# Optimization experiments

Hardware: AMD Instinct MI355X
Metric: run time of the kernel (lower is better)

The kernel has to match this reference:

```python
import jax, jax.numpy as jnp
import numpy as np

HEADS = 8
DIM_HEAD = 64
CHUNK = 128
EPS = 1e-6
KERNEL_EPS = 1e-4


def softmax_kernel(x, proj, is_query):
    # x: [b,h,n,d], proj: [f,d]  (FAVOR+ positive softmax features)
    d = x.shape[-1]
    data_normalizer = d ** -0.25
    ratio = proj.shape[0] ** -0.5
    data_dash = jnp.einsum('bhnd,fd->bhnf', x * data_normalizer, proj)
    diag = 0.5 * (data_normalizer ** 2) * jnp.sum(x * x, axis=-1, keepdims=True)  # [b,h,n,1]
    if is_query:
        m = jnp.max(data_dash, axis=-1, keepdims=True)
    else:
        m = jnp.max(data_dash, axis=(-1, -2), keepdims=True)
    return ratio * (jnp.exp(data_dash - diag - jax.lax.stop_gradient(m)) + KERNEL_EPS)


def infer_hidden_states(q, k, v, chunk_size=CHUNK):
    # q,k: [b,h,n,f], v: [b,h,n,e]; chunked causal linear attention with carried cumsums
    b, h, n, f = q.shape
    e = v.shape[-1]
    nc = n // chunk_size

    def to_chunks(t):
        return jnp.moveaxis(t.reshape(b, h, nc, chunk_size, t.shape[-1]), 2, 0)

    qs, ks, vs = to_chunks(q), to_chunks(k), to_chunks(v)

    def step(carry, inp):
        Z, S = carry  # [b,h,1,f], [b,h,1,f,e]
        qc, kc, vc = inp
        k_cum = Z + jnp.cumsum(kc, axis=2)                       # [b,h,c,f]
        D_inv = 1.0 / jnp.einsum('bhnf,bhnf->bhn', qc, k_cum + EPS)
        ctx = jnp.einsum('bhnf,bhne->bhnfe', kc, vc)             # [b,h,c,f,e]
        ctx_cum = S + jnp.cumsum(ctx, axis=2)
        out = jnp.einsum('bhnfe,bhnf,bhn->bhne', ctx_cum, qc, D_inv)
        return (k_cum[:, :, -1:], ctx_cum[:, :, -1:]), out

    init = (jnp.zeros((b, h, 1, f), q.dtype), jnp.zeros((b, h, 1, f, e), q.dtype))
    (Z, S), outs = jax.lax.scan(step, init, (qs, ks, vs))
    out = jnp.moveaxis(outs, 0, 2).reshape(b, h, n, e)
    return out, Z[:, :, 0], S[:, :, 0]


def reference(x, proj, Wq, Wk, Wv, Wo, bo):
    b, n, dim = x.shape
    h, dh = HEADS, DIM_HEAD

    def split_heads(t):
        return jnp.transpose(t.reshape(b, n, h, dh), (0, 2, 1, 3))

    q = split_heads(x @ Wq)
    k = split_heads(x @ Wk)
    v = split_heads(x @ Wv)

    qf = softmax_kernel(q, proj, is_query=True)
    kf = softmax_kernel(k, proj, is_query=False)

    out, Z, S = infer_hidden_states(qf, kf, v)
    out = jnp.transpose(out, (0, 2, 1, 3)).reshape(b, n, h * dh)
    out = out @ Wo + bo
    return out, Z, S


def setup_inputs() -> dict:
    key = jax.random.key(0)
    ks = jax.random.split(key, 6)
    b, n, dim = 2, 2048, 512
    f = 256
    return {
        'x': jax.random.normal(ks[0], (b, n, dim), jnp.float32),
        'proj': jax.random.normal(ks[1], (f, DIM_HEAD), jnp.float32),
        'Wq': jax.random.normal(ks[2], (dim, dim), jnp.float32) * (dim ** -0.5),
        'Wk': jax.random.normal(ks[3], (dim, dim), jnp.float32) * (dim ** -0.5),
        'Wv': jax.random.normal(ks[4], (dim, dim), jnp.float32) * (dim ** -0.5),
        'Wo': jax.random.normal(ks[5], (dim, dim), jnp.float32) * (dim ** -0.5),
        'bo': jnp.zeros((dim,), jnp.float32),
    }
```

## Files before the change

### kernel.cpp

```cpp
#include <hip/hip_runtime.h>
#include <hip/hip_bf16.h>
#include <math.h>

#define NB    2
#define NSEQ  2048
#define DIMM  512
#define NH    8
#define DHd   64
#define FF    256
#define CHK   128
#define NCHK  16
#define NBH   16

typedef unsigned short ushort_t;
typedef __attribute__((ext_vector_type(8))) __bf16 bf16x8;
typedef __attribute__((ext_vector_type(4))) float floatx4;

__device__ __forceinline__ unsigned short f2bf(float x) {
    union { __hip_bfloat16 h; unsigned short u; } v;
    v.h = __float2bfloat16(x);
    return v.u;
}
__device__ __forceinline__ float bf2f(unsigned short u) {
    union { unsigned short u2[2]; float f; } v;
    v.u2[0] = 0; v.u2[1] = u;
    return v.f;
}
__device__ __forceinline__ unsigned enc_f(float x) {
    unsigned u = __float_as_uint(x);
    return (u & 0x80000000u) ? ~u : (u | 0x80000000u);
}
__device__ __forceinline__ float dec_f(unsigned e) {
    unsigned u = (e & 0x80000000u) ? (e & 0x7fffffffu) : ~e;
    return __uint_as_float(u);
}

__device__ __forceinline__ void gload16(const void* g, void* l) {
    __builtin_amdgcn_global_load_lds(
        (const __attribute__((address_space(1))) void*)g,
        (__attribute__((address_space(3))) void*)l, 16, 0, 0);
}

__device__ __forceinline__ bf16x8 frag8(const ushort_t* lds, int row, int kb) {
    return *((const bf16x8*)lds + row * 8 + (kb ^ (row & 7)));
}
__device__ __forceinline__ bf16x8 fragS(const ushort_t* lds, int row, int kb) {
    return *((const bf16x8*)lds + row * 16 + (kb ^ (row & 15)));
}

__device__ __forceinline__ void stage8(const ushort_t* __restrict__ G, ushort_t* dst,
                                       int ld, int tid) {
#pragma unroll
    for (int t = 0; t < 4; t++) {
        const int g = t * 256 + tid, r = g >> 3, kb = (g & 7) ^ (r & 7);
        gload16(G + (size_t)r * ld + kb * 8, dst + (size_t)g * 8);
    }
}
__device__ __forceinline__ void stage4h(const ushort_t* __restrict__ G, ushort_t* dst,
                                        int ld, int tid) {
#pragma unroll
    for (int t = 0; t < 2; t++) {
        const int g = t * 256 + tid, r = g >> 3, kb = (g & 7) ^ (r & 7);
        gload16(G + (size_t)r * ld + kb * 8, dst + (size_t)g * 8);
    }
}
__device__ __forceinline__ void stageV(const ushort_t* __restrict__ G, ushort_t* dst,
                                       int tid) {
#pragma unroll
    for (int t = 0; t < 4; t++) {
        const int g = t * 256 + tid, r = g >> 4, kb = (g & 15) ^ (r & 15);
        gload16(G + (size_t)r * NSEQ + kb * 8, dst + (size_t)g * 8);
    }
}

__global__ __launch_bounds__(256)
void prep(const float* __restrict__ x, const float* __restrict__ proj,
          const float* __restrict__ W0, const float* __restrict__ W1,
          const float* __restrict__ W2, const float* __restrict__ W3,
          ushort_t* __restrict__ xb, ushort_t* __restrict__ projb,
          ushort_t* __restrict__ T0, ushort_t* __restrict__ T1,
          ushort_t* __restrict__ T2, ushort_t* __restrict__ T3,
          unsigned* __restrict__ mk_u)
{
    __shared__ float t[32][33];
    const int b = blockIdx.x, tid = threadIdx.x;
    if (b < 2048) {
        const int gid = b * 256 + tid;
        const float4 v = *(const float4*)(x + (size_t)gid * 4);
        union { ushort4 v4; unsigned short s[4]; } pk;
        pk.s[0] = f2bf(v.x); pk.s[1] = f2bf(v.y); pk.s[2] = f2bf(v.z); pk.s[3] = f2bf(v.w);
        ((ushort4*)xb)[gid] = pk.v4;
    } else if (b < 2064) {
        const int gid = (b - 2048) * 256 + tid;
        const float dn = 0.35355339059327379f;
        const float4 v = *(const float4*)(proj + (size_t)gid * 4);
        union { ushort4 v4; unsigned short s[4]; } pk;
        pk.s[0] = f2bf(v.x * dn); pk.s[1] = f2bf(v.y * dn);
        pk.s[2] = f2bf(v.z * dn); pk.s[3] = f2bf(v.w * dn);
        ((ushort4*)projb)[gid] = pk.v4;
    } else if (b < 3088) {
        const int idx = b - 2064;
        const int z = idx >> 8, rem = idx & 255;
        const int bx = rem & 15, by = rem >> 4;
        const float* W = (z == 0) ? W0 : (z == 1) ? W1 : (z == 2) ? W2 : W3;
        ushort_t* T = (z == 0) ? T0 : (z == 1) ? T1 : (z == 2) ? T2 : T3;
        const int x0 = bx * 32, y0 = by * 32;
        const int tx = tid & 31, ty = tid >> 5;
#pragma unroll
        for (int i = 0; i < 4; i++)
            t[ty + i * 8][tx] = W[(size_t)(y0 + ty + i * 8) * DIMM + x0 + tx];
        __syncthreads();
#pragma unroll
        for (int i = 0; i < 4; i++)
            T[(size_t)(x0 + ty + i * 8) * DIMM + y0 + tx] = f2bf(t[tx][ty + i * 8]);
    } else {
        if (tid < NBH) mk_u[tid] = 0u;
    }
}

__device__ __forceinline__ void mfma_mainloop(
    const ushort_t* __restrict__ AG, const ushort_t* __restrict__ BG,
    ushort_t* As, ushort_t* Bs, int ldA, int ldB, int K,
    floatx4 acc[4][4], int tid)
{
    const int lane = tid & 63, wid = tid >> 6;
    const int q = lane >> 4, c = lane & 15;
    const int wm = (wid >> 1) * 64, wn = (wid & 1) * 64;

    for (int k0 = 0; k0 < K; k0 += 64) {
#pragma unroll
        for (int t = 0; t < 4; t++) {
            const int g = t * 256 + tid, r = g >> 3, kb = (g & 7) ^ (r & 7);
            gload16(AG + (size_t)r * ldA + k0 + kb * 8, As + (size_t)g * 8);
        }
#pragma unroll
        for (int t = 0; t < 4; t++) {
            const int g = t * 256 + tid, r = g >> 3, kb = (g & 7) ^ (r & 7);
            gload16(BG + (size_t)r * ldB + k0 + kb * 8, Bs + (size_t)g * 8);
        }
        __syncthreads();
#pragma unroll
        for (int ks = 0; ks < 2; ks++) {
            bf16x8 af[4], bfr[4];
#pragma unroll
            for (int i = 0; i < 4; i++) {
                af[i]  = frag8(As, wm + i * 16 + c, ks * 4 + q);
                bfr[i] = frag8(Bs, wn + i * 16 + c, ks * 4 + q);
            }
#pragma unroll
            for (int i = 0; i < 4; i++)
#pragma unroll
                for (int j = 0; j < 4; j++)
                    acc[i][j] = __builtin_amdgcn_mfma_f32_16x16x32_bf16(
                        af[i], bfr[j], acc[i][j], 0, 0, 0);
        }
        __syncthreads();
    }
}

__global__ __launch_bounds__(256)
void gemm_qkv(const ushort_t* __restrict__ xb,
              const ushort_t* __restrict__ Wtq, const ushort_t* __restrict__ Wtk,
              const ushort_t* __restrict__ Wtv, const ushort_t* __restrict__ projb,
              ushort_t* __restrict__ qb, ushort_t* __restrict__ kb,
              ushort_t* __restrict__ vTb, unsigned* __restrict__ mk_u)
{
    __shared__ alignas(16) ushort_t SM[25600];
    __shared__ float red[256];
    ushort_t* As = SM;
    ushort_t* Bs = SM + 8192;
    ushort_t* PS = SM + 17408;
    const int tid = threadIdx.x;
    const int bid = blockIdx.x;
    const int z = bid % 3, tt = bid / 3;
    const int n0 = (tt & 3) * 128, m0 = (tt >> 2) * 128;
    const ushort_t* Bt = (z == 0) ? Wtq : ((z == 1) ? Wtk : Wtv);

    floatx4 zero = {0.f, 0.f, 0.f, 0.f};
    floatx4 acc[4][4];
#pragma unroll
    for (int i = 0; i < 4; i++)
#pragma unroll
        for (int j = 0; j < 4; j++) acc[i][j] = zero;

    mfma_mainloop(xb + (size_t)m0 * DIMM, Bt + (size_t)n0 * DIMM, As, Bs,
                  DIMM, DIMM, DIMM, acc, tid);

    const int lane = tid & 63, wid = tid >> 6;
    const int q = lane >> 4, cl = lane & 15;
    const int wm = (wid >> 1) * 64, wn = (wid & 1) * 64;

#pragma unroll
    for (int i = 0; i < 4; i++)
#pragma unroll
        for (int j = 0; j < 4; j++) {
            const int col = wn + j * 16 + cl;
#pragma unroll
            for (int r = 0; r < 4; r++) {
                const int row = wm + i * 16 + q * 4 + r;
                SM[row * 136 + col] = f2bf(acc[i][j][r]);
            }
        }
    __syncthreads();

    if (z < 2) {
        ushort_t* ob = (z == 0) ? qb : kb;
        if (z == 1) {
#pragma unroll
            for (int t = 0; t < 4; t++) {
                const int g = t * 256 + tid, f = g >> 3, kbg = (g & 7) ^ (f & 7);
                gload16(projb + (size_t)f * 64 + kbg * 8, PS + (size_t)g * 8);
            }
        }
#pragma unroll
        for (int p = 0; p < 16; p++) {
            const int idx = p * 256 + tid;
            const int row = idx >> 5, c4 = idx & 31;
            ushort4 o = *(const ushort4*)&SM[row * 136 + c4 * 4];
            *(ushort4*)(ob + (size_t)(m0 + row) * DIMM + n0 + c4 * 4) = o;
        }
        if (z == 1) {
            const int bb = m0 >> 11;
            const int h0 = n0 >> 6;
            float mx[2] = {-3.0e38f, -3.0e38f};
#pragma unroll
            for (int half = 0; half < 2; half++) {
                __syncthreads();
#pragma unroll
                for (int hh = 0; hh < 2; hh++) {
                    floatx4 a2[4][4];
#pragma unroll
                    for (int i = 0; i < 4; i++)
#pragma unroll
                        for (int j = 0; j < 4; j++) a2[i][j] = zero;
#pragma unroll
                    for (int ks = 0; ks < 2; ks++) {
                        bf16x8 af[4], bfr[4];
#pragma unroll
                        for (int i = 0; i < 4; i++)
                            af[i] = *(const bf16x8*)&SM[(wm + i * 16 + cl) * 136 + hh * 64 + (ks * 4 + q) * 8];
#pragma unroll
                        for (int j = 0; j < 4; j++)
                            bfr[j] = frag8(PS, wn + j * 16 + cl, ks * 4 + q);
#pragma unroll
                        for (int i = 0; i < 4; i++)
#pragma unroll
                            for (int j = 0; j < 4; j++)
                                a2[i][j] = __builtin_amdgcn_mfma_f32_16x16x32_bf16(
                                    af[i], bfr[j], a2[i][j], 0, 0, 0);
                    }
#pragma unroll
                    for (int i = 0; i < 4; i++)
#pragma unroll
                        for (int j = 0; j < 4; j++)
#pragma unroll
                            for (int r = 0; r < 4; r++) mx[hh] = fmaxf(mx[hh], a2[i][j][r]);
                }
                if (half == 0) {
                    __syncthreads();
#pragma unroll
                    for (int t = 0; t < 4; t++) {
                        const int g = t * 256 + tid, f = g >> 3, kbg = (g & 7) ^ (f & 7);
                        gload16(projb + (size_t)(128 + f) * 64 + kbg * 8, PS + (size_t)g * 8);
                    }
                }
            }
#pragma unroll
            for (int hh = 0; hh < 2; hh++) {
                __syncthreads();
                red[tid] = mx[hh];
                __syncthreads();
                for (int s = 128; s > 0; s >>= 1) {
                    if (tid < s) red[tid] = fmaxf(red[tid], red[tid + s]);
                    __syncthreads();
                }
                if (tid == 0) atomicMax(&mk_u[bb * NH + h0 + hh], enc_f(red[0]));
            }
        }
    } else {
        const int bb = m0 >> 11, nbase = m0 & 2047;
#pragma unroll
        for (int p = 0; p < 16; p++) {
            const int idx = p * 256 + tid;
            const int cl2 = idx >> 5, n4 = idx & 31;
            const int C = n0 + cl2;
            const int h = C >> 6, e = C & 63;
            union { ushort4 v4; unsigned short s[4]; } pk;
#pragma unroll
            for (int k = 0; k < 4; k++) pk.s[k] = SM[(n4 * 4 + k) * 136 + cl2];
            *(ushort4*)(vTb + (((size_t)(bb * NH + h) * 64 + e)) * NSEQ + nbase + n4 * 4) = pk.v4;
        }
    }
}

__global__ __launch_bounds__(256)
void gemm_out(const ushort_t* __restrict__ attnb, const ushort_t* __restrict__ Wto,
              float* __restrict__ out, const float* __restrict__ bias)
{
    __shared__ alignas(16) ushort_t As[4096];
    __shared__ alignas(16) ushort_t Bs[8192];
    const int tid = threadIdx.x;
    const int n0 = blockIdx.x * 128, m0 = blockIdx.y * 64;
    const ushort_t* AG = attnb + (size_t)m0 * DIMM;
    const ushort_t* BG = Wto + (size_t)n0 * DIMM;

    floatx4 zero = {0.f, 0.f, 0.f, 0.f};
    floatx4 acc[2][4];
#pragma unroll
    for (int i = 0; i < 2; i++)
#pragma unroll
        for (int j = 0; j < 4; j++) acc[i][j] = zero;

    const int lane = tid & 63, wid = tid >> 6;
    const int q = lane >> 4, c = lane & 15;
    const int wm = (wid >> 1) * 32, wn = (wid & 1) * 64;

    for (int k0 = 0; k0 < DIMM; k0 += 64) {
        stage4h(AG + k0, As, DIMM, tid);
        stage8(BG + k0, Bs, DIMM, tid);
        __syncthreads();
#pragma unroll
        for (int ks = 0; ks < 2; ks++) {
            bf16x8 af[2], bfr[4];
#pragma unroll
            for (int i = 0; i < 2; i++) af[i] = frag8(As, wm + i * 16 + c, ks * 4 + q);
#pragma unroll
            for (int j = 0; j < 4; j++) bfr[j] = frag8(Bs, wn + j * 16 + c, ks * 4 + q);
#pragma unroll
            for (int i = 0; i < 2; i++)
#pragma unroll
                for (int j = 0; j < 4; j++)
                    acc[i][j] = __builtin_amdgcn_mfma_f32_16x16x32_bf16(
                        af[i], bfr[j], acc[i][j], 0, 0, 0);
        }
        __syncthreads();
    }

#pragma unroll
    for (int i = 0; i < 2; i++)
#pragma unroll
        for (int j = 0; j < 4; j++) {
            const int col = n0 + wn + j * 16 + c;
            const float bv = bias[col];
#pragma unroll
            for (int r = 0; r < 4; r++) {
                const int row = m0 + wm + i * 16 + q * 4 + r;
                out[(size_t)row * DIMM + col] = acc[i][j][r] + bv;
            }
        }
}

__global__ __launch_bounds__(256)
void featk(const ushort_t* __restrict__ kb_, const ushort_t* __restrict__ projb,
           const unsigned* __restrict__ mk_u, const ushort_t* __restrict__ vTb,
           ushort_t* __restrict__ kfb, float* __restrict__ CTXT,
           float* __restrict__ Ksum)
{
    __shared__ alignas(16) ushort_t SM[17408];
    __shared__ alignas(16) ushort_t Vs[8192];
    __shared__ float dtmp[256];
    __shared__ float diag_l[128];
    __shared__ float colp[2][128];
    ushort_t* As = SM;
    ushort_t* Bs = SM + 8192;
    const int tid = threadIdx.x, lane = tid & 63, wid = tid >> 6;
    const int q = lane >> 4, cl = lane & 15;
    const int m0 = blockIdx.x * 128, h = blockIdx.y, fh = blockIdx.z;
    const int bb = m0 >> 11, nloc = m0 & 2047;
    const int bh = bb * NH + h;
    const int cidx = nloc >> 7;
    const ushort_t* Aq = kb_ + (size_t)m0 * DIMM + h * 64;
    const ushort_t* Vg = vTb + ((size_t)bh * 64) * NSEQ + nloc;
    const ushort_t* Pj = projb + (size_t)fh * 128 * 64;

    {
        const int row = tid >> 1, half = tid & 1;
        float s = 0.f;
        const ushort_t* p = Aq + (size_t)row * DIMM + half * 32;
#pragma unroll
        for (int d = 0; d < 32; d += 4) {
            ushort4 w = *(const ushort4*)(p + d);
            float a = bf2f(w.x), b2 = bf2f(w.y), c2 = bf2f(w.z), d2 = bf2f(w.w);
            s += a * a + b2 * b2 + c2 * c2 + d2 * d2;
        }
        dtmp[tid] = s;
    }
    stage8(Aq, As, DIMM, tid);
    stage8(Pj, Bs, 64, tid);
    stageV(Vg, Vs, tid);
    __syncthreads();
    if (tid < 128) diag_l[tid] = (dtmp[2 * tid] + dtmp[2 * tid + 1]) * 0.0625f;

    floatx4 zero = {0.f, 0.f, 0.f, 0.f};
    floatx4 acc[4][4];
#pragma unroll
    for (int i = 0; i < 4; i++)
#pragma unroll
        for (int j = 0; j < 4; j++) acc[i][j] = zero;
    const int wm = (wid >> 1) * 64, wn = (wid & 1) * 64;
#pragma unroll
    for (int ks = 0; ks < 2; ks++) {
        bf16x8 af[4], bfr[4];
#pragma unroll
        for (int i = 0; i < 4; i++) af[i] = frag8(As, wm + i * 16 + cl, ks * 4 + q);
#pragma unroll
        for (int j = 0; j < 4; j++) bfr[j] = frag8(Bs, wn + j * 16 + cl, ks * 4 + q);
#pragma unroll
        for (int i = 0; i < 4; i++)
#pragma unroll
            for (int j = 0; j < 4; j++)
                acc[i][j] = __builtin_amdgcn_mfma_f32_16x16x32_bf16(
                    af[i], bfr[j], acc[i][j], 0, 0, 0);
    }
    __syncthreads();

    const float mk = dec_f(mk_u[bh]);
#pragma unroll
    for (int i = 0; i < 4; i++)
#pragma unroll
        for (int r = 0; r < 4; r++) {
            const int row = wm + i * 16 + q * 4 + r;
            const float cc = diag_l[row] + mk;
#pragma unroll
            for (int j = 0; j < 4; j++)
                acc[i][j][r] = 0.0625f * (__expf(acc[i][j][r] - cc) + 1.0e-4f);
        }

#pragma unroll
    for (int j = 0; j < 4; j++) {
        float s = 0.f;
#pragma unroll
        for (int i = 0; i < 4; i++)
            s += acc[i][j][0] + acc[i][j][1] + acc[i][j][2] + acc[i][j][3];
        s += __shfl_xor(s, 16);
        s += __shfl_xor(s, 32);
        if (q == 0) colp[wid >> 1][wn + j * 16 + cl] = s;
    }

#pragma unroll
    for (int i = 0; i < 4; i++)
#pragma unroll
        for (int j = 0; j < 4; j++) {
            const int col = wn + j * 16 + cl;
#pragma unroll
            for (int r = 0; r < 4; r++) {
                const int row = wm + i * 16 + q * 4 + r;
                SM[row * 136 + col] = f2bf(acc[i][j][r]);
            }
        }
    __syncthreads();

    if (tid < 128)
        Ksum[((size_t)bh * NCHK + cidx) * FF + fh * 128 + tid] = colp[0][tid] + colp[1][tid];

    const size_t frow = (size_t)bh * NSEQ + nloc;
#pragma unroll
    for (int p = 0; p < 16; p++) {
        const int idx = p * 256 + tid;
        const int row = idx >> 5, c4 = idx & 31;
        ushort4 o = *(const ushort4*)&SM[row * 136 + c4 * 4];
        *(ushort4*)(kfb + (frow + row) * FF + fh * 128 + c4 * 4) = o;
    }
    __syncthreads();

    ushort_t* T = SM;
    const size_t cbase = ((size_t)bh * NCHK + cidx) * 64;
#pragma unroll
    for (int fq = 0; fq < 2; fq++) {
        if ((wid & 1) == fq) {
#pragma unroll
            for (int jj = 0; jj < 4; jj++) {
#pragma unroll
                for (int i = 0; i < 4; i++)
#pragma unroll
                    for (int r = 0; r < 4; r++) {
                        const int n = wm + i * 16 + q * 4 + r;
                        T[(jj * 16 + cl) * 136 + n] = f2bf(acc[i][jj][r]);
                    }
            }
        }
        __syncthreads();
        floatx4 accc[4];
#pragma unroll
        for (int jj = 0; jj < 4; jj++) accc[jj] = zero;
#pragma unroll
        for (int kt = 0; kt < 4; kt++) {
            const bf16x8 av = fragS(Vs, wid * 16 + cl, kt * 4 + q);
#pragma unroll
            for (int jj = 0; jj < 4; jj++) {
                const bf16x8 bv = *(const bf16x8*)(T + (jj * 16 + cl) * 136 + (kt * 4 + q) * 8);
                accc[jj] = __builtin_amdgcn_mfma_f32_16x16x32_bf16(av, bv, accc[jj], 0, 0, 0);
            }
        }
#pragma unroll
        for (int jj = 0; jj < 4; jj++) {
            const int f = fh * 128 + fq * 64 + jj * 16 + cl;
#pragma unroll
            for (int r = 0; r < 4; r++) {
                const int e = wid * 16 + q * 4 + r;
                CTXT[(cbase + e) * FF + f] = accc[jj][r];
            }
        }
        __syncthreads();
    }
}

__global__ void prefix_zs(float* __restrict__ Ksum, float* __restrict__ Zout,
                          const float* __restrict__ CTXT, ushort_t* __restrict__ ctxp,
                          float* __restrict__ Sout)
{
    const int b = blockIdx.x;
    if (b < 1024) {
        const int idx = b * 256 + threadIdx.x;
        const int bh = idx >> 14, ef = idx & 16383;
        const int e = ef >> 8, f = ef & 255;
        float run = 0.f;
#pragma unroll
        for (int c = 0; c < NCHK; c++) {
            const size_t o = (((size_t)bh * NCHK + c) * 64 + e) * FF + f;
            const float t = CTXT[o];
            ctxp[o] = f2bf(run);
            run += t;
        }
        Sout[((size_t)bh * FF + f) * 64 + e] = run;
    } else {
        const int idx = (b - 1024) * 256 + threadIdx.x;
        const int bh = idx >> 8, f = idx & 255;
        float run = 0.f;
#pragma unroll
        for (int c = 0; c < NCHK; c++) {
            const size_t o = ((size_t)(bh * NCHK + c)) * FF + f;
            const float t = Ksum[o];
            Ksum[o] = run;
            run += t;
        }
        Zout[(size_t)bh * FF + f] = run;
    }
}

template<int NJ>
__device__ __forceinline__ void st1N(const ushort_t* QFs, const ushort_t* Bk,
                                     floatx4* acc1, int wv, int cl, int q)
{
#pragma unroll
    for (int ks = 0; ks < 2; ks++) {
        const bf16x8 af = frag8(QFs, wv * 16 + cl, ks * 4 + q);
        bf16x8 bfr[NJ];
#pragma unroll
        for (int j = 0; j < NJ; j++) bfr[j] = frag8(Bk, j * 16 + cl, ks * 4 + q);
#pragma unroll
        for (int j = 0; j < NJ; j++)
            acc1[j] = __builtin_amdgcn_mfma_f32_16x16x32_bf16(af, bfr[j], acc1[j], 0, 0, 0);
    }
}

__device__ __forceinline__ void pv4(const ushort_t* CpB, const ushort_t* QFs,
                                    floatx4 acc2[4], int wv, int cl, int q)
{
#pragma unroll
    for (int ks = 0; ks < 2; ks++) {
        const bf16x8 bfr = frag8(QFs, wv * 16 + cl, ks * 4 + q);
#pragma unroll
        for (int i = 0; i < 4; i++) {
            const bf16x8 af = frag8(CpB, i * 16 + cl, ks * 4 + q);
            acc2[i] = __builtin_amdgcn_mfma_f32_16x16x32_bf16(af, bfr, acc2[i], 0, 0, 0);
        }
    }
}

__global__ __launch_bounds__(256)
void chunk_out_half(const ushort_t* __restrict__ qb_, const ushort_t* __restrict__ projb,
                    const ushort_t* __restrict__ kfb, const ushort_t* __restrict__ vTb,
                    const float* __restrict__ Zex, const ushort_t* __restrict__ ctxp,
                    ushort_t* __restrict__ attnb)
{
    __shared__ alignas(16) ushort_t QF[16384];
    __shared__ alignas(16) ushort_t BufA[8192];
    __shared__ alignas(16) ushort_t Ssl[8192];
    __shared__ alignas(16) ushort_t BufB[4096];
    __shared__ float zeps[256];
    __shared__ float dtmp[256];
    __shared__ float diag_l[64];
    __shared__ float rows_part[64];
    __shared__ float denp[256];
    __shared__ float den_l[64];

    const int tid = threadIdx.x, lane = tid & 63, wv = tid >> 6;
    const int q = lane >> 4, cl = lane & 15;
    const int bh = blockIdx.x >> 5, r5 = blockIdx.x & 31;
    const int c = r5 >> 1, hq = r5 & 1;
    const int bb = bh >> 3, h = bh & 7;
    const int n0 = c * CHK, q0 = n0 + hq * 64;
    const ushort_t* Kf = kfb + ((size_t)bh * NSEQ + n0) * FF;
    const ushort_t* Aq = qb_ + ((size_t)(bb * NSEQ + q0)) * DIMM + h * 64;
    const ushort_t* Vt = vTb + ((size_t)bh * 64) * NSEQ + n0;
    const ushort_t* Cp = ctxp + ((size_t)bh * NCHK + c) * 64 * FF;

    zeps[tid] = Zex[((size_t)bh * NCHK + c) * FF + tid] + 1.0e-6f;

    stage4h(Aq, BufB, DIMM, tid);
    stage8(projb, BufA, 64, tid);
    stage8(projb + 128 * 64, Ssl, 64, tid);
    {
        const int row = tid >> 2, qd = tid & 3;
        float s = 0.f;
        const ushort_t* p = Aq + (size_t)row * DIMM + qd * 16;
#pragma unroll
        for (int d = 0; d < 16; d += 4) {
            ushort4 w = *(const ushort4*)(p + d);
            float a = bf2f(w.x), b2 = bf2f(w.y), c2 = bf2f(w.z), d2 = bf2f(w.w);
            s += a * a + b2 * b2 + c2 * c2 + d2 * d2;
        }
        dtmp[tid] = s;
    }
    __syncthreads();
    if (tid < 64)
        diag_l[tid] = (dtmp[4 * tid] + dtmp[4 * tid + 1] +
                       dtmp[4 * tid + 2] + dtmp[4 * tid + 3]) * 0.0625f;

    floatx4 zero = {0.f, 0.f, 0.f, 0.f};
    floatx4 accqA[8], accqB[8];
#pragma unroll
    for (int j = 0; j < 8; j++) { accqA[j] = zero; accqB[j] = zero; }
#pragma unroll
    for (int ks = 0; ks < 2; ks++) {
        const bf16x8 af = frag8(BufB, wv * 16 + cl, ks * 4 + q);
#pragma unroll
        for (int j = 0; j < 8; j++) {
            const bf16x8 b0 = frag8(BufA, j * 16 + cl, ks * 4 + q);
            accqA[j] = __builtin_amdgcn_mfma_f32_16x16x32_bf16(af, b0, accqA[j], 0, 0, 0);
        }
#pragma unroll
        for (int j = 0; j < 8; j++) {
            const bf16x8 b1 = frag8(Ssl, j * 16 + cl, ks * 4 + q);
            accqB[j] = __builtin_amdgcn_mfma_f32_16x16x32_bf16(af, b1, accqB[j], 0, 0, 0);
        }
    }
    float rmax[4];
#pragma unroll
    for (int r = 0; r < 4; r++) {
        float m = -3.0e38f;
#pragma unroll
        for (int j = 0; j < 8; j++) m = fmaxf(m, fmaxf(accqA[j][r], accqB[j][r]));
        m = fmaxf(m, __shfl_xor(m, 1)); m = fmaxf(m, __shfl_xor(m, 2));
        m = fmaxf(m, __shfl_xor(m, 4)); m = fmaxf(m, __shfl_xor(m, 8));
        rmax[r] = m;
    }
    __syncthreads();
#pragma unroll
    for (int r = 0; r < 4; r++) {
        const int rowL = wv * 16 + q * 4 + r;
        const float cc = diag_l[rowL] + rmax[r];
#pragma unroll
        for (int j = 0; j < 8; j++) {
            {
                const int col = j * 16 + cl;
                const float v = 0.0625f * (__expf(accqA[j][r] - cc) + 1.0e-4f);
                const int s = col >> 6, fp = col & 63;
                QF[s * 4096 + (rowL * 8 + ((fp >> 3) ^ (rowL & 7))) * 8 + (fp & 7)] = f2bf(v);
            }
            {
                const int col = 128 + j * 16 + cl;
                const float v = 0.0625f * (__expf(accqB[j][r] - cc) + 1.0e-4f);
                const int s = col >> 6, fp = col & 63;
                QF[s * 4096 + (rowL * 8 + ((fp >> 3) ^ (rowL & 7))) * 8 + (fp & 7)] = f2bf(v);
            }
        }
    }
    if (hq) stage8(Kf, Ssl, FF, tid); else stage4h(Kf, Ssl, FF, tid);
    __syncthreads();

    floatx4 acc1[8];
#pragma unroll
    for (int j = 0; j < 8; j++) acc1[j] = zero;
    if (hq) {
        stage8(Kf + 64, BufA, FF, tid);
        st1N<8>(QF, Ssl, acc1, wv, cl, q);
        __syncthreads();
        stage8(Kf + 128, Ssl, FF, tid);
        st1N<8>(QF + 4096, BufA, acc1, wv, cl, q);
        __syncthreads();
        stage8(Kf + 192, BufA, FF, tid);
        st1N<8>(QF + 8192, Ssl, acc1, wv, cl, q);
        __syncthreads();
        st1N<8>(QF + 12288, BufA, acc1, wv, cl, q);
    } else {
        stage4h(Kf + 64, BufA, FF, tid);
        st1N<4>(QF, Ssl, acc1, wv, cl, q);
        __syncthreads();
        stage4h(Kf + 128, Ssl, FF, tid);
        st1N<4>(QF + 4096, BufA, acc1, wv, cl, q);
        __syncthreads();
        stage4h(Kf + 192, BufA, FF, tid);
        st1N<4>(QF + 8192, Ssl, acc1, wv, cl, q);
        __syncthreads();
        st1N<4>(QF + 12288, BufA, acc1, wv, cl, q);
    }

    if (hq) {
#pragma unroll
        for (int r = 0; r < 4; r++) {
            const int rowL = wv * 16 + q * 4 + r;
            const int rowG = 64 + rowL;
            float part = 0.f;
#pragma unroll
            for (int j = 0; j < 8; j++) {
                const int col = j * 16 + cl;
                const float v = (col <= rowG) ? acc1[j][r] : 0.f;
                part += v;
                Ssl[(rowL * 16 + ((col >> 3) ^ (rowL & 15))) * 8 + (col & 7)] = f2bf(v);
            }
            part += __shfl_xor(part, 1); part += __shfl_xor(part, 2);
            part += __shfl_xor(part, 4); part += __shfl_xor(part, 8);
            if (cl == 0) rows_part[rowL] = part;
        }
    } else {
#pragma unroll
        for (int r = 0; r < 4; r++) {
            const int rowL = wv * 16 + q * 4 + r;
            float part = 0.f;
#pragma unroll
            for (int j = 0; j < 4; j++) {
                const int col = j * 16 + cl;
                const float v = (col <= rowL) ? acc1[j][r] : 0.f;
                part += v;
                Ssl[(rowL * 16 + ((col >> 3) ^ (rowL & 15))) * 8 + (col & 7)] = f2bf(v);
            }
            part += __shfl_xor(part, 1); part += __shfl_xor(part, 2);
            part += __shfl_xor(part, 4); part += __shfl_xor(part, 8);
            if (cl == 0) rows_part[rowL] = part;
        }
    }
    __syncthreads();

    if (hq) stageV(Vt, BufA, tid); else stage4h(Vt, BufA, NSEQ, tid);
    stage4h(Cp, BufB, FF, tid);
    float dacc = 0.f;
    {
        const int drow = tid >> 2, dq = tid & 3;
        const ushort_t* QQ = QF + dq * 4096;
#pragma unroll
        for (int gi = 0; gi < 8; gi++) {
            const ushort_t* gp = QQ + ((size_t)drow * 8 + (gi ^ (drow & 7))) * 8;
            const int kbase = dq * 64 + gi * 8;
#pragma unroll
            for (int e2 = 0; e2 < 8; e2++)
                dacc = fmaf(bf2f(gp[e2]), zeps[kbase + e2], dacc);
        }
    }
    __syncthreads();

    floatx4 acc2[4];
#pragma unroll
    for (int i = 0; i < 4; i++) acc2[i] = zero;
    if (hq) {
#pragma unroll
        for (int kk = 0; kk < 4; kk++) {
            const bf16x8 bfr = fragS(Ssl, wv * 16 + cl, kk * 4 + q);
#pragma unroll
            for (int i = 0; i < 4; i++) {
                const bf16x8 af = fragS(BufA, i * 16 + cl, kk * 4 + q);
                acc2[i] = __builtin_amdgcn_mfma_f32_16x16x32_bf16(af, bfr, acc2[i], 0, 0, 0);
            }
        }
    } else {
#pragma unroll
        for (int kk = 0; kk < 2; kk++) {
            const bf16x8 bfr = fragS(Ssl, wv * 16 + cl, kk * 4 + q);
#pragma unroll
            for (int i = 0; i < 4; i++) {
                const bf16x8 af = frag8(BufA, i * 16 + cl, kk * 4 + q);
                acc2[i] = __builtin_amdgcn_mfma_f32_16x16x32_bf16(af, bfr, acc2[i], 0, 0, 0);
            }
        }
    }
    denp[tid] = dacc;
    __syncthreads();

    stage4h(Cp + 64, BufA, FF, tid);
    stage4h(Cp + 128, BufA + 4096, FF, tid);
    pv4(BufB, QF, acc2, wv, cl, q);
    __syncthreads();
    stage4h(Cp + 192, BufB, FF, tid);
    pv4(BufA, QF + 4096, acc2, wv, cl, q);
    pv4(BufA + 4096, QF + 8192, acc2, wv, cl, q);
    if (tid < 64)
        den_l[tid] = rows_part[tid] + denp[4 * tid] + denp[4 * tid + 1] +
                     denp[4 * tid + 2] + denp[4 * tid + 3];
    __syncthreads();
    pv4(BufB, QF + 12288, acc2, wv, cl, q);

    const float dinv = 1.0f / den_l[wv * 16 + cl];
#pragma unroll
    for (int i = 0; i < 4; i++)
#pragma unroll
        for (int r = 0; r < 4; r++) {
            const int e = i * 16 + q * 4 + r;
            Ssl[(wv * 16 + cl) * 68 + e] = f2bf(acc2[i][r] * dinv);
        }
    __syncthreads();
#pragma unroll
    for (int p = 0; p < 4; p++) {
        const int idx = p * 256 + tid;
        const int row = idx >> 4, e4 = idx & 15;
        ushort4 o = *(const ushort4*)&Ssl[row * 68 + e4 * 4];
        *(ushort4*)(attnb + ((size_t)(bb * NSEQ + q0 + row)) * DIMM + h * 64 + e4 * 4) = o;
    }
}

extern "C" void kernel_launch(void* const* d_in, const int* in_sizes, int n_in,
                              void* d_out, int out_size, void* d_ws, size_t ws_size,
                              hipStream_t stream)
{
    (void)in_sizes; (void)n_in; (void)out_size; (void)ws_size;
    const float* x    = (const float*)d_in[0];
    const float* proj = (const float*)d_in[1];
    const float* Wq   = (const float*)d_in[2];
    const float* Wk   = (const float*)d_in[3];
    const float* Wv   = (const float*)d_in[4];
    const float* Wo   = (const float*)d_in[5];
    const float* bo   = (const float*)d_in[6];
    float* out = (float*)d_out;

    char* W = (char*)d_ws;
    float*    CTXT = (float*)W;              W += (size_t)16777216;
    ushort_t* kfb  = (ushort_t*)W;           W += (size_t)16777216;
    ushort_t* ctxp = (ushort_t*)W;           W += (size_t)8388608;
    ushort_t* qb   = (ushort_t*)W;           W += (size_t)4194304;
    ushort_t* kb   = (ushort_t*)W;           W += (size_t)4194304;
    ushort_t* xb   = (ushort_t*)W;           W += (size_t)4194304;
    ushort_t* vTb  = (ushort_t*)W;           W += (size_t)4194304;
    ushort_t* Wtq  = (ushort_t*)W;           W += (size_t)524288;
    ushort_t* Wtk  = (ushort_t*)W;           W += (size_t)524288;
    ushort_t* Wtv  = (ushort_t*)W;           W += (size_t)524288;
    ushort_t* Wto  = (ushort_t*)W;           W += (size_t)524288;
    ushort_t* projb = (ushort_t*)W;          W += (size_t)32768;
    float*    Ksum = (float*)W;              W += (size_t)262144;
    unsigned* mk_u = (unsigned*)W;           W += (size_t)256;

    ushort_t* attnb = xb;

    float* Zout = out + (size_t)4096 * 512;
    float* Sout = Zout + (size_t)NBH * FF;

    hipLaunchKernelGGL(prep, dim3(3089), dim3(256), 0, stream,
                       x, proj, Wq, Wk, Wv, Wo, xb, projb, Wtq, Wtk, Wtv, Wto, mk_u);
    hipLaunchKernelGGL(gemm_qkv, dim3(384), dim3(256), 0, stream,
                       xb, Wtq, Wtk, Wtv, projb, qb, kb, vTb, mk_u);
    hipLaunchKernelGGL(featk, dim3(32, 8, 2), dim3(256), 0, stream,
                       kb, projb, mk_u, vTb, kfb, CTXT, Ksum);
    hipLaunchKernelGGL(prefix_zs, dim3(1040), dim3(256), 0, stream,
                       Ksum, Zout, CTXT, ctxp, Sout);
    hipLaunchKernelGGL(chunk_out_half, dim3(512), dim3(256), 0, stream,
                       qb, projb, kfb, vTb, Ksum, ctxp, attnb);
    hipLaunchKernelGGL(gemm_out, dim3(4, 64), dim3(256), 0, stream, attnb, Wto, out, bo);
}
```

Measured before the change: 136.0 us.

## Split key-max reduction into separate kernel and double-buffer output GEMM

Moves the global key-feature max computation out of the gemm_qkv epilogue into a dedicated kmax kernel launched over (row tile, head, feature half). It uses wave shuffles instead of a shared-memory tree reduction. This removes the serialized tail and extra LDS from the z==1 QKV blocks, so those blocks no longer run longer than the q and v blocks. It also double-buffers the gemm_out K-loop so global loads overlap MFMA work. The cost is one more kernel launch and rereading kb from global memory.

```diff
diff --git a/kernel.cpp b/kernel.cpp
--- a/kernel.cpp
+++ b/kernel.cpp
@@ -161,15 +161,13 @@
 __global__ __launch_bounds__(256)
 void gemm_qkv(const ushort_t* __restrict__ xb,
               const ushort_t* __restrict__ Wtq, const ushort_t* __restrict__ Wtk,
-              const ushort_t* __restrict__ Wtv, const ushort_t* __restrict__ projb,
+              const ushort_t* __restrict__ Wtv,
               ushort_t* __restrict__ qb, ushort_t* __restrict__ kb,
-              ushort_t* __restrict__ vTb, unsigned* __restrict__ mk_u)
-{
-    __shared__ alignas(16) ushort_t SM[25600];
-    __shared__ float red[256];
+              ushort_t* __restrict__ vTb)
+{
+    __shared__ alignas(16) ushort_t SM[17408];
     ushort_t* As = SM;
     ushort_t* Bs = SM + 8192;
-    ushort_t* PS = SM + 17408;
     const int tid = threadIdx.x;
     const int bid = blockIdx.x;
     const int z = bid % 3, tt = bid / 3;
@@ -205,77 +203,12 @@
 
     if (z < 2) {
         ushort_t* ob = (z == 0) ? qb : kb;
-        if (z == 1) {
-#pragma unroll
-            for (int t = 0; t < 4; t++) {
-                const int g = t * 256 + tid, f = g >> 3, kbg = (g & 7) ^ (f & 7);
-                gload16(projb + (size_t)f * 64 + kbg * 8, PS + (size_t)g * 8);
-            }
-        }
 #pragma unroll
         for (int p = 0; p < 16; p++) {
             const int idx = p * 256 + tid;
             const int row = idx >> 5, c4 = idx & 31;
             ushort4 o = *(const ushort4*)&SM[row * 136 + c4 * 4];
             *(ushort4*)(ob + (size_t)(m0 + row) * DIMM + n0 + c4 * 4) = o;
-        }
-        if (z == 1) {
-            const int bb = m0 >> 11;
-            const int h0 = n0 >> 6;
-            float mx[2] = {-3.0e38f, -3.0e38f};
-#pragma unroll
-            for (int half = 0; half < 2; half++) {
-                __syncthreads();
-#pragma unroll
-                for (int hh = 0; hh < 2; hh++) {
-                    floatx4 a2[4][4];
-#pragma unroll
-                    for (int i = 0; i < 4; i++)
-#pragma unroll
-                        for (int j = 0; j < 4; j++) a2[i][j] = zero;
-#pragma unroll
-                    for (int ks = 0; ks < 2; ks++) {
-                        bf16x8 af[4], bfr[4];
-#pragma unroll
-                        for (int i = 0; i < 4; i++)
-                            af[i] = *(const bf16x8*)&SM[(wm + i * 16 + cl) * 136 + hh * 64 + (ks * 4 + q) * 8];
-#pragma unroll
-                        for (int j = 0; j < 4; j++)
-                            bfr[j] = frag8(PS, wn + j * 16 + cl, ks * 4 + q);
-#pragma unroll
-                        for (int i = 0; i < 4; i++)
-#pragma unroll
-                            for (int j = 0; j < 4; j++)
-                                a2[i][j] = __builtin_amdgcn_mfma_f32_16x16x32_bf16(
-                                    af[i], bfr[j], a2[i][j], 0, 0, 0);
-                    }
-#pragma unroll
-                    for (int i = 0; i < 4; i++)
-#pragma unroll
-                        for (int j = 0; j < 4; j++)
-#pragma unroll
-                            for (int r = 0; r < 4; r++) mx[hh] = fmaxf(mx[hh], a2[i][j][r]);
-                }
-                if (half == 0) {
-                    __syncthreads();
-#pragma unroll
-                    for (int t = 0; t < 4; t++) {
-                        const int g = t * 256 + tid, f = g >> 3, kbg = (g & 7) ^ (f & 7);
-                        gload16(projb + (size_t)(128 + f) * 64 + kbg * 8, PS + (size_t)g * 8);
-                    }
-                }
-            }
-#pragma unroll
-            for (int hh = 0; hh < 2; hh++) {
-                __syncthreads();
-                red[tid] = mx[hh];
-                __syncthreads();
-                for (int s = 128; s > 0; s >>= 1) {
-                    if (tid < s) red[tid] = fmaxf(red[tid], red[tid + s]);
-                    __syncthreads();
-                }
-                if (tid == 0) atomicMax(&mk_u[bb * NH + h0 + hh], enc_f(red[0]));
-            }
         }
     } else {
         const int bb = m0 >> 11, nbase = m0 & 2047;
@@ -294,11 +227,90 @@
 }
 
 __global__ __launch_bounds__(256)
+void kmax(const ushort_t* __restrict__ kb_, const ushort_t* __restrict__ projb,
+          unsigned* __restrict__ mk_u)
+{
+    __shared__ alignas(16) ushort_t As[8192];
+    __shared__ alignas(16) ushort_t Bs[8192];
+    __shared__ float wred[4];
+    const int tid = threadIdx.x, lane = tid & 63, wid = tid >> 6;
+    const int q = lane >> 4, cl = lane & 15;
+    const int m0 = blockIdx.x * 128, h = blockIdx.y, fh = blockIdx.z;
+    const int bb = m0 >> 11;
+    const int bh = bb * NH + h;
+    const ushort_t* Aq = kb_ + (size_t)m0 * DIMM + h * 64;
+
+    stage8(Aq, As, DIMM, tid);
+    stage8(projb + (size_t)fh * 128 * 64, Bs, 64, tid);
+    __syncthreads();
+
+    floatx4 zero = {0.f, 0.f, 0.f, 0.f};
+    floatx4 acc[4][4];
+#pragma unroll
+    for (int i = 0; i < 4; i++)
+#pragma unroll
+        for (int j = 0; j < 4; j++) acc[i][j] = zero;
+    const int wm = (wid >> 1) * 64, wn = (wid & 1) * 64;
+#pragma unroll
+    for (int ks = 0; ks < 2; ks++) {
+        bf16x8 af[4], bfr[4];
+#pragma unroll
+        for (int i = 0; i < 4; i++) af[i] = frag8(As, wm + i * 16 + cl, ks * 4 + q);
+#pragma unroll
+        for (int j = 0; j < 4; j++) bfr[j] = frag8(Bs, wn + j * 16 + cl, ks * 4 + q);
+#pragma unroll
+        for (int i = 0; i < 4; i++)
+#pragma unroll
+            for (int j = 0; j < 4; j++)
+                acc[i][j] = __builtin_amdgcn_mfma_f32_16x16x32_bf16(
+                    af[i], bfr[j], acc[i][j], 0, 0, 0);
+    }
+
+    float mx = -3.0e38f;
+#pragma unroll
+    for (int i = 0; i < 4; i++)
+#pragma unroll
+        for (int j = 0; j < 4; j++)
+#pragma unroll
+            for (int r = 0; r < 4; r++) mx = fmaxf(mx, acc[i][j][r]);
+    mx = fmaxf(mx, __shfl_xor(mx, 1));  mx = fmaxf(mx, __shfl_xor(mx, 2));
+    mx = fmaxf(mx, __shfl_xor(mx, 4));  mx = fmaxf(mx, __shfl_xor(mx, 8));
+    mx = fmaxf(mx, __shfl_xor(mx, 16)); mx = fmaxf(mx, __shfl_xor(mx, 32));
+    if (lane == 0) wred[wid] = mx;
+    __syncthreads();
+    if (tid == 0) {
+        const float m = fmaxf(fmaxf(wred[0], wred[1]), fmaxf(wred[2], wred[3]));
+        atomicMax(&mk_u[bh], enc_f(m));
+    }
+}
+
+__device__ __forceinline__ void mm24(const ushort_t* A, const ushort_t* B,
+                                     floatx4 acc[2][4], int wm, int wn, int c, int q)
+{
+#pragma unroll
+    for (int ks = 0; ks < 2; ks++) {
+        bf16x8 af[2], bfr[4];
+#pragma unroll
+        for (int i = 0; i < 2; i++) af[i] = frag8(A, wm + i * 16 + c, ks * 4 + q);
+#pragma unroll
+        for (int j = 0; j < 4; j++) bfr[j] = frag8(B, wn + j * 16 + c, ks * 4 + q);
+#pragma unroll
+        for (int i = 0; i < 2; i++)
+#pragma unroll
+            for (int j = 0; j < 4; j++)
+                acc[i][j] = __builtin_amdgcn_mfma_f32_16x16x32_bf16(
+                    af[i], bfr[j], acc[i][j], 0, 0, 0);
+    }
+}
+
+__global__ __launch_bounds__(256)
 void gemm_out(const ushort_t* __restrict__ attnb, const ushort_t* __restrict__ Wto,
               float* __restrict__ out, const float* __restrict__ bias)
 {
-    __shared__ alignas(16) ushort_t As[4096];
-    __shared__ alignas(16) ushort_t Bs[8192];
+    __shared__ alignas(16) ushort_t A0[4096];
+    __shared__ alignas(16) ushort_t A1[4096];
+    __shared__ alignas(16) ushort_t B0[8192];
+    __shared__ alignas(16) ushort_t B1[8192];
     const int tid = threadIdx.x;
     const int n0 = blockIdx.x * 128, m0 = blockIdx.y * 64;
     const ushort_t* AG = attnb + (size_t)m0 * DIMM;
@@ -315,24 +327,20 @@
     const int q = lane >> 4, c = lane & 15;
     const int wm = (wid >> 1) * 32, wn = (wid & 1) * 64;
 
-    for (int k0 = 0; k0 < DIMM; k0 += 64) {
-        stage4h(AG + k0, As, DIMM, tid);
-        stage8(BG + k0, Bs, DIMM, tid);
-        __syncthreads();
-#pragma unroll
-        for (int ks = 0; ks < 2; ks++) {
-            bf16x8 af[2], bfr[4];
-#pragma unroll
-            for (int i = 0; i < 2; i++) af[i] = frag8(As, wm + i * 16 + c, ks * 4 + q);
-#pragma unroll
-            for (int j = 0; j < 4; j++) bfr[j] = frag8(Bs, wn + j * 16 + c, ks * 4 + q);
-#pragma unroll
-            for (int i = 0; i < 2; i++)
-#pragma unroll
-                for (int j = 0; j < 4; j++)
-                    acc[i][j] = __builtin_amdgcn_mfma_f32_16x16x32_bf16(
-                        af[i], bfr[j], acc[i][j], 0, 0, 0);
-        }
+    stage4h(AG, A0, DIMM, tid);
+    stage8(BG, B0, DIMM, tid);
+    __syncthreads();
+    for (int tt = 0; tt < 4; tt++) {
+        const int k0 = tt * 128;
+        stage4h(AG + k0 + 64, A1, DIMM, tid);
+        stage8(BG + k0 + 64, B1, DIMM, tid);
+        mm24(A0, B0, acc, wm, wn, c, q);
+        __syncthreads();
+        if (tt < 3) {
+            stage4h(AG + k0 + 128, A0, DIMM, tid);
+            stage8(BG + k0 + 128, B0, DIMM, tid);
+        }
+        mm24(A1, B1, acc, wm, wn, c, q);
         __syncthreads();
     }
 
@@ -846,7 +854,9 @@
     hipLaunchKernelGGL(prep, dim3(3089), dim3(256), 0, stream,
                        x, proj, Wq, Wk, Wv, Wo, xb, projb, Wtq, Wtk, Wtv, Wto, mk_u);
     hipLaunchKernelGGL(gemm_qkv, dim3(384), dim3(256), 0, stream,
-                       xb, Wtq, Wtk, Wtv, projb, qb, kb, vTb, mk_u);
+                       xb, Wtq, Wtk, Wtv, qb, kb, vTb);
+    hipLaunchKernelGGL(kmax, dim3(32, 8, 2), dim3(256), 0, stream,
+                       kb, projb, mk_u);
     hipLaunchKernelGGL(featk, dim3(32, 8, 2), dim3(256), 0, stream,
                        kb, projb, mk_u, vTb, kfb, CTXT, Ksum);
     hipLaunchKernelGGL(prefix_zs, dim3(1040), dim3(256), 0, stream,
```

Result: slower. 142.1 us (+4.5%).
